# Kernel tuning notes

Measured on AMD Instinct MI355X. Metric: run time of the kernel, lower is better.

## Reference

```python
import jax, jax.numpy as jnp
import numpy as np

NUM_HEADS = 16
ROPE_THETA = 10000.0


def _rope(x, pos):
    # x: [B, H, S, d_k], pos: [S]
    d_k = x.shape[-1]
    inv_freq = ROPE_THETA ** (-jnp.arange(0, d_k, 2, dtype=x.dtype) / d_k)  # [d_k/2]
    ang = pos[:, None].astype(x.dtype) * inv_freq[None, :]  # [S, d_k/2]
    cos, sin = jnp.cos(ang), jnp.sin(ang)
    x1 = x[..., 0::2]
    x2 = x[..., 1::2]
    r1 = x1 * cos - x2 * sin
    r2 = x1 * sin + x2 * cos
    return jnp.stack([r1, r2], axis=-1).reshape(x.shape)


def setup_inputs() -> dict:
    key = jax.random.key(0)
    kx, kq, kk, kv = jax.random.split(key, 4)
    B, S, D = 2, 2048, 2048
    scale = 1.0 / np.sqrt(D)
    x = jax.random.normal(kx, (B, S, D), dtype=jnp.float32)
    wq = jax.random.normal(kq, (D, D), dtype=jnp.float32) * scale
    wk = jax.random.normal(kk, (D, D), dtype=jnp.float32) * scale
    wv = jax.random.normal(kv, (D, D), dtype=jnp.float32) * scale
    return {"x": x, "wq": wq, "wk": wk, "wv": wv}


def reference(x, wq, wk, wv):
    B, S, D = x.shape
    H = NUM_HEADS
    d_k = D // H
    # QKV projections (Linear stores weight as [out, in]; y = x @ W^T)
    q = (x @ wq.T).reshape(B, S, H, d_k).transpose(0, 2, 1, 3)  # [B,H,S,dk]
    k = (x @ wk.T).reshape(B, S, H, d_k).transpose(0, 2, 1, 3)
    v = (x @ wv.T).reshape(B, S, H, d_k).transpose(0, 2, 1, 3)
    pos = jnp.arange(S)
    q = _rope(q, pos)
    k = _rope(k, pos)
    scores = jnp.einsum("bhqd,bhkd->bhqk", q, k) / jnp.sqrt(jnp.asarray(d_k, x.dtype))
    causal = jnp.tril(jnp.ones((S, S), dtype=bool))
    scores = jnp.where(causal, scores, jnp.asarray(-1e9, x.dtype))
    attn = jax.nn.softmax(scores, axis=-1)
    out = jnp.einsum("bhqk,bhkd->bhqd", attn, v)  # [B,H,S,dk]
    return out.transpose(0, 2, 1, 3).reshape(B, S, D)
```

## Files before the change

kernel.cpp:

```cpp
#include <hip/hip_runtime.h>
#include <stdint.h>

typedef unsigned short u16;
typedef __bf16 bf16x8 __attribute__((ext_vector_type(8)));
typedef float f32x4 __attribute__((ext_vector_type(4)));

#define NHEADS 16
#define DKH    128
#define SEQ    2048
#define DMODEL 2048
#define NBATCH 2

typedef const __attribute__((address_space(1))) void* gas1_t;
typedef __attribute__((address_space(3))) void* las3_t;

__device__ __forceinline__ void gload_lds16(const void* g, void* l) {
  __builtin_amdgcn_global_load_lds((gas1_t)(uintptr_t)g,
                                   (las3_t)(uint32_t)(uintptr_t)l, 16, 0, 0);
}

__device__ __forceinline__ u16 bf(float f) {
  return __builtin_bit_cast(u16, (__bf16)f);
}

__global__ __launch_bounds__(256) void cvt_all(const float* __restrict__ x,
                                               const float* __restrict__ wq,
                                               const float* __restrict__ wk,
                                               const float* __restrict__ wv,
                                               u16* __restrict__ xb,
                                               u16* __restrict__ wb) {
  int i = (blockIdx.x * 256 + threadIdx.x) * 4;
  const int NX = NBATCH * SEQ * DMODEL;
  const int NW = DMODEL * DMODEL;
  const float* src;
  u16* dst;
  int j;
  if (i < NX) { src = x; dst = xb; j = i; }
  else {
    int k = i - NX;
    int w = k / NW;
    j = k - w * NW;
    src = (w == 0) ? wq : (w == 1) ? wk : wv;
    dst = wb + (size_t)w * NW;
  }
  const float4 v = *(const float4*)(src + j);
  uint2 o;
  o.x = (uint32_t)bf(v.x) | ((uint32_t)bf(v.y) << 16);
  o.y = (uint32_t)bf(v.z) | ((uint32_t)bf(v.w) << 16);
  *(uint2*)(dst + j) = o;
}

__global__ __launch_bounds__(256) void rope_table(float2* __restrict__ tbl) {
  int i = blockIdx.x * 256 + threadIdx.x;
  int s = i >> 6, d2 = i & 63;
  const float kLog2Theta = 13.28771237954945f;
  float inv_freq = exp2f(-(float)d2 * (2.0f / 128.0f) * kLog2Theta);
  float ang = (float)s * inv_freq;
  tbl[i] = make_float2(cosf(ang), sinf(ang));
}

__global__ __launch_bounds__(256, 4) void gemm_qkv(const u16* __restrict__ Abf,
                                                   const u16* __restrict__ Wbf,
                                                   const float2* __restrict__ rope,
                                                   u16* __restrict__ qb,
                                                   u16* __restrict__ kb,
                                                   u16* __restrict__ vtb) {
  __shared__ u16 S[16384];
  u16* As = S;
  u16* Bs = S + 8192;
  const int tid = threadIdx.x;
  const int lane = tid & 63, wid = tid >> 6;
  const int wr = wid >> 1, wc = wid & 1;
  const int blk = blockIdx.x;
  const int m0 = (blk / 48) * 128;
  const int n0 = (blk % 48) * 128;
  const int lrow = lane & 15, lgrp = lane >> 4, lko = lgrp * 8;
  const int rswz = (lrow & 7) << 3;

  const int srow = tid >> 3;
  const int scol = ((tid & 7) * 8) ^ (((tid >> 3) & 7) << 3);

  f32x4 acc[4][4] = {};

  for (int k0 = 0; k0 < DMODEL; k0 += 64) {
    __syncthreads();
#pragma unroll
    for (int c = 0; c < 4; ++c) {
      gload_lds16(Abf + (size_t)(m0 + c * 32 + srow) * DMODEL + k0 + scol,
                  As + (c * 256 + tid) * 8);
      gload_lds16(Wbf + (size_t)(n0 + c * 32 + srow) * DMODEL + k0 + scol,
                  Bs + (c * 256 + tid) * 8);
    }
    __syncthreads();
#pragma unroll
    for (int kk = 0; kk < 2; ++kk) {
      const int rc = (kk * 32 + lko) ^ rswz;
      bf16x8 a[4], b[4];
#pragma unroll
      for (int m = 0; m < 4; ++m)
        a[m] = *(const bf16x8*)(As + (wr * 64 + m * 16 + lrow) * 64 + rc);
#pragma unroll
      for (int n = 0; n < 4; ++n)
        b[n] = *(const bf16x8*)(Bs + (wc * 64 + n * 16 + lrow) * 64 + rc);
#pragma unroll
      for (int m = 0; m < 4; ++m)
#pragma unroll
        for (int n = 0; n < 4; ++n)
          acc[m][n] = __builtin_amdgcn_mfma_f32_16x16x32_bf16(a[m], b[n], acc[m][n], 0, 0, 0);
    }
  }

  const int sel = n0 >> 11;
  const float qsc = 0.08838834764831845f * 1.44269504088896341f;

  if (sel != 2) {
#pragma unroll
    for (int m = 0; m < 4; ++m) {
      int grow0 = m0 + wr * 64 + m * 16 + (lgrp << 2);
#pragma unroll
      for (int n = 0; n < 4; ++n) {
        int gcol = n0 + wc * 64 + n * 16 + lrow;
        int within = gcol & 2047;
        int h_ = within >> 7, d_ = within & 127;
#pragma unroll
        for (int j = 0; j < 4; ++j) {
          float v = acc[m][n][j];
          int r = grow0 + j;
          int b_ = r >> 11, s_ = r & 2047;
          int bh = b_ * NHEADS + h_;
          float part = __shfl_xor(v, 1);
          float2 cs2 = rope[s_ * 64 + (d_ >> 1)];
          v = (d_ & 1) ? (part * cs2.y + v * cs2.x) : (v * cs2.x - part * cs2.y);
          if (sel == 0) v *= qsc;
          u16* dq = sel ? kb : qb;
          dq[((size_t)bh * SEQ + s_) * DKH + d_] = bf(v);
        }
      }
    }
  } else {
    __syncthreads();
#pragma unroll
    for (int m = 0; m < 4; ++m) {
      int sl0 = wr * 64 + m * 16 + (lgrp << 2);
#pragma unroll
      for (int n = 0; n < 4; ++n) {
        int dcol = wc * 64 + n * 16 + lrow;
        const int dx = (dcol & 7) << 4;
#pragma unroll
        for (int j = 0; j < 4; ++j)
          S[dcol * 128 + ((sl0 + j) ^ dx)] = bf(acc[m][n][j]);
      }
    }
    __syncthreads();
    const int b_ = m0 >> 11, s0 = m0 & 2047;
    const int h_ = (n0 >> 7) & 15;
    const int bh = b_ * NHEADS + h_;
    const int d = tid >> 1, hf = tid & 1;
    const int dx = (d & 7) << 4;
    u16* grow = vtb + ((size_t)bh * DKH + d) * SEQ + s0 + hf * 64;
#pragma unroll
    for (int g = 0; g < 8; ++g) {
      bf16x8 v8 = *(const bf16x8*)(S + d * 128 + ((hf * 64 + g * 8) ^ dx));
      *(bf16x8*)(grow + g * 8) = v8;
    }
  }
}

__global__ __launch_bounds__(256, 2) void attn_fwd(const u16* __restrict__ qb,
                                                   const u16* __restrict__ kb,
                                                   const u16* __restrict__ vtb,
                                                   float* __restrict__ out) {
  __shared__ u16 Ks[2][64 * 128];
  __shared__ u16 Vs[2][128 * 64];
  __shared__ __bf16 Ps[4][16 * 64];
  const int tid = threadIdx.x, lane = tid & 63, wid = tid >> 6;
  const int blk = blockIdx.x;
  const int xcd = blk & 7, slot = blk >> 3;
  const int bh = (slot >> 4) * 8 + xcd;
  const int pair = slot & 15;
  const int lrow = lane & 15, lgrp = lane >> 4, lko = lgrp * 8;
  const int swz = (lrow & 7) << 3;

  const int krow_l = tid >> 4;
  const int kcol = ((tid & 15) * 8) ^ ((krow_l & 7) << 3);
  const int vrow_l = tid >> 3;
  const int vcol = ((tid & 7) * 8) ^ ((vrow_l & 7) << 3);

  const int b_ = bh >> 4, h_ = bh & 15;
  const size_t kbase = (size_t)bh * SEQ;
  const size_t vbase = (size_t)bh * DKH;

#pragma unroll 1
  for (int ci = 0; ci < 2; ++ci) {
    const int chunk = ci ? (31 - pair) : pair;
    const int qrow0 = chunk * 64 + wid * 16;

    bf16x8 qa[4];
#pragma unroll
    for (int kd = 0; kd < 4; ++kd)
      qa[kd] = *(const bf16x8*)(qb + (kbase + qrow0 + lrow) * DKH + kd * 32 + lko);

    f32x4 o[8] = {};
    float mrun[4], lrun[4];
#pragma unroll
    for (int j = 0; j < 4; ++j) { mrun[j] = -1e30f; lrun[j] = 0.f; }

    const int nt = chunk + 1;

#pragma unroll
    for (int c = 0; c < 4; ++c) {
      gload_lds16(kb + (kbase + c * 16 + krow_l) * DKH + kcol,
                  &Ks[0][(c * 256 + tid) * 8]);
      gload_lds16(vtb + (vbase + c * 32 + vrow_l) * SEQ + vcol,
                  &Vs[0][(c * 256 + tid) * 8]);
    }
    __syncthreads();

#pragma unroll 1
    for (int t = 0; t < nt; ++t) {
      const int cur = t & 1;
      if (t + 1 < nt) {
        const int kv1 = (t + 1) * 64;
#pragma unroll
        for (int c = 0; c < 4; ++c) {
          gload_lds16(kb + (kbase + kv1 + c * 16 + krow_l) * DKH + kcol,
                      &Ks[cur ^ 1][(c * 256 + tid) * 8]);
          gload_lds16(vtb + (vbase + c * 32 + vrow_l) * SEQ + kv1 + vcol,
                      &Vs[cur ^ 1][(c * 256 + tid) * 8]);
        }
      }
      const int kv0 = t * 64;
      const u16* Kb = &Ks[cur][0];
      const u16* Vb = &Vs[cur][0];

      f32x4 sf[4] = {};
      __builtin_amdgcn_s_setprio(1);
#pragma unroll
      for (int kd = 0; kd < 4; ++kd) {
        const int kc = (kd * 32 + lko) ^ swz;
#pragma unroll
        for (int n = 0; n < 4; ++n) {
          bf16x8 kf = *(const bf16x8*)(Kb + (n * 16 + lrow) * 128 + kc);
          sf[n] = __builtin_amdgcn_mfma_f32_16x16x32_bf16(qa[kd], kf, sf[n], 0, 0, 0);
        }
      }
      __builtin_amdgcn_s_setprio(0);

      const bool diag = (t == nt - 1);
      float mt[4];
#pragma unroll
      for (int j = 0; j < 4; ++j) {
        const int r = qrow0 + lgrp * 4 + j;
        float m_ = -1e30f;
#pragma unroll
        for (int n = 0; n < 4; ++n) {
          float s = sf[n][j];
          if (diag && (kv0 + n * 16 + lrow > r)) { s = -1e30f; sf[n][j] = s; }
          m_ = fmaxf(m_, s);
        }
#pragma unroll
        for (int off = 1; off < 16; off <<= 1) m_ = fmaxf(m_, __shfl_xor(m_, off));
        mt[j] = m_;
      }
      int need = 0;
#pragma unroll
      for (int j = 0; j < 4; ++j) need |= (mt[j] > mrun[j] + 11.5f) ? 1 : 0;
      if (__any(need)) {
#pragma unroll
        for (int j = 0; j < 4; ++j) {
          float mnew = fmaxf(mrun[j], mt[j]);
          float alpha = __builtin_amdgcn_exp2f(mrun[j] - mnew);
          mrun[j] = mnew;
          lrun[j] *= alpha;
#pragma unroll
          for (int n8 = 0; n8 < 8; ++n8) o[n8][j] *= alpha;
        }
      }
#pragma unroll
      for (int j = 0; j < 4; ++j) {
        float ps = 0.f;
#pragma unroll
        for (int n = 0; n < 4; ++n) {
          float p = __builtin_amdgcn_exp2f(sf[n][j] - mrun[j]);
          ps += p;
          sf[n][j] = p;
        }
#pragma unroll
        for (int off = 1; off < 16; off <<= 1) ps += __shfl_xor(ps, off);
        lrun[j] += ps;
      }

      __bf16* pw = &Ps[wid][0];
#pragma unroll
      for (int n = 0; n < 4; ++n)
#pragma unroll
        for (int j = 0; j < 4; ++j) {
          int prow = lgrp * 4 + j;
          pw[prow * 64 + ((n * 16 + lrow) ^ ((prow & 7) << 3))] = (__bf16)sf[n][j];
        }

      __builtin_amdgcn_s_setprio(1);
#pragma unroll
      for (int kk = 0; kk < 2; ++kk) {
        const int pc = (kk * 32 + lko) ^ swz;
        bf16x8 pa = *(const bf16x8*)(pw + lrow * 64 + pc);
#pragma unroll
        for (int n = 0; n < 8; ++n) {
          bf16x8 vf = *(const bf16x8*)(Vb + (n * 16 + lrow) * 64 + pc);
          o[n] = __builtin_amdgcn_mfma_f32_16x16x32_bf16(pa, vf, o[n], 0, 0, 0);
        }
      }
      __builtin_amdgcn_s_setprio(0);

      __syncthreads();
    }

#pragma unroll
    for (int j = 0; j < 4; ++j) {
      int s_ = qrow0 + lgrp * 4 + j;
      float inv = 1.f / lrun[j];
#pragma unroll
      for (int n = 0; n < 8; ++n) {
        int dcol = n * 16 + lrow;
        out[((size_t)b_ * SEQ + s_) * DMODEL + h_ * DKH + dcol] = o[n][j] * inv;
      }
    }
  }
}

extern "C" void kernel_launch(void* const* d_in, const int* in_sizes, int n_in,
                              void* d_out, int out_size, void* d_ws, size_t ws_size,
                              hipStream_t stream) {
  const float* x  = (const float*)d_in[0];
  const float* wq = (const float*)d_in[1];
  const float* wk = (const float*)d_in[2];
  const float* wv = (const float*)d_in[3];
  float* out = (float*)d_out;
  char* ws = (char*)d_ws;

  u16* xb  = (u16*)(ws);
  u16* wb  = (u16*)(ws + 16777216);
  u16* qb  = (u16*)(ws + 41943040);
  u16* kb  = (u16*)(ws + 58720256);
  u16* vtb = (u16*)(ws + 75497472);

  float2* rope = (float2*)d_out;

  rope_table<<<512, 256, 0, stream>>>(rope);
  cvt_all<<<20480, 256, 0, stream>>>(x, wq, wk, wv, xb, wb);
  gemm_qkv<<<1536, 256, 0, stream>>>(xb, wb, rope, qb, kb, vtb);
  attn_fwd<<<512, 256, 0, stream>>>(qb, kb, vtb, out);
}
```

Measured before the change: 216.5 us.

## Rewrite attention with 32x32x16 MFMA, 32 query rows per wave, register-resident P

The attention kernel now uses 32x32x16 bf16 MFMA and computes S transposed, so each lane owns one query row. That makes the row max and sum mostly in-register with one cross-half shuffle. P is packed to bf16 and exchanged between lane halves with shuffles instead of going through LDS. Each block now handles 128 query rows, so the grid is halved and occupancy drops to one block per CU. The XCD-aware head mapping is removed. The aim is fewer LDS round-trips and reductions per tile, at the cost of more registers and fewer resident waves.

```diff
diff --git a/kernel.cpp b/kernel.cpp
--- a/kernel.cpp
+++ b/kernel.cpp
@@ -4,6 +4,7 @@
 typedef unsigned short u16;
 typedef __bf16 bf16x8 __attribute__((ext_vector_type(8)));
 typedef float f32x4 __attribute__((ext_vector_type(4)));
+typedef float f32x16 __attribute__((ext_vector_type(16)));
 
 #define NHEADS 16
 #define DKH    128
@@ -21,6 +22,15 @@
 
 __device__ __forceinline__ u16 bf(float f) {
   return __builtin_bit_cast(u16, (__bf16)f);
+}
+
+__device__ __forceinline__ uint32_t pk(float lo, float hi) {
+  return (uint32_t)bf(lo) | ((uint32_t)bf(hi) << 16);
+}
+
+__device__ __forceinline__ float lanebcast(int srclane, float v) {
+  return __builtin_bit_cast(float,
+      __builtin_amdgcn_ds_bpermute(srclane << 2, __builtin_bit_cast(int, v)));
 }
 
 __global__ __launch_bounds__(256) void cvt_all(const float* __restrict__ x,
@@ -166,166 +176,169 @@
   }
 }
 
-__global__ __launch_bounds__(256, 2) void attn_fwd(const u16* __restrict__ qb,
+__global__ __launch_bounds__(256, 1) void attn_fwd(const u16* __restrict__ qb,
                                                    const u16* __restrict__ kb,
                                                    const u16* __restrict__ vtb,
                                                    float* __restrict__ out) {
   __shared__ u16 Ks[2][64 * 128];
   __shared__ u16 Vs[2][128 * 64];
-  __shared__ __bf16 Ps[4][16 * 64];
   const int tid = threadIdx.x, lane = tid & 63, wid = tid >> 6;
   const int blk = blockIdx.x;
-  const int xcd = blk & 7, slot = blk >> 3;
-  const int bh = (slot >> 4) * 8 + xcd;
-  const int pair = slot & 15;
-  const int lrow = lane & 15, lgrp = lane >> 4, lko = lgrp * 8;
-  const int swz = (lrow & 7) << 3;
+  const int bh = blk & 31;
+  const int pair = blk >> 5;
+  const int qln = lane & 31, hi = lane >> 5;
+  const int hi4 = hi << 2, hi8 = hi << 3;
+  const int kswz = (qln & 15) << 3;
+  const int vswz = (qln & 7) << 3;
 
   const int krow_l = tid >> 4;
-  const int kcol = ((tid & 15) * 8) ^ ((krow_l & 7) << 3);
+  const int kcol = (((tid & 15) ^ (tid >> 4)) << 3);
   const int vrow_l = tid >> 3;
-  const int vcol = ((tid & 7) * 8) ^ ((vrow_l & 7) << 3);
+  const int vcol = (((tid & 7) ^ ((tid >> 3) & 7)) << 3);
 
   const int b_ = bh >> 4, h_ = bh & 15;
   const size_t kbase = (size_t)bh * SEQ;
   const size_t vbase = (size_t)bh * DKH;
 
+#define STAGE_KV(bufi, kv_)                                                  \
+  _Pragma("unroll")                                                          \
+  for (int c = 0; c < 4; ++c) {                                              \
+    gload_lds16(kb + (kbase + (kv_) + c * 16 + krow_l) * DKH + kcol,         \
+                &Ks[bufi][(c * 256 + tid) * 8]);                             \
+    gload_lds16(vtb + (vbase + c * 32 + vrow_l) * SEQ + (kv_) + vcol,        \
+                &Vs[bufi][(c * 256 + tid) * 8]);                             \
+  }
+
 #pragma unroll 1
   for (int ci = 0; ci < 2; ++ci) {
-    const int chunk = ci ? (31 - pair) : pair;
-    const int qrow0 = chunk * 64 + wid * 16;
-
-    bf16x8 qa[4];
-#pragma unroll
-    for (int kd = 0; kd < 4; ++kd)
-      qa[kd] = *(const bf16x8*)(qb + (kbase + qrow0 + lrow) * DKH + kd * 32 + lko);
-
-    f32x4 o[8] = {};
-    float mrun[4], lrun[4];
-#pragma unroll
-    for (int j = 0; j < 4; ++j) { mrun[j] = -1e30f; lrun[j] = 0.f; }
-
-    const int nt = chunk + 1;
-
-#pragma unroll
-    for (int c = 0; c < 4; ++c) {
-      gload_lds16(kb + (kbase + c * 16 + krow_l) * DKH + kcol,
-                  &Ks[0][(c * 256 + tid) * 8]);
-      gload_lds16(vtb + (vbase + c * 32 + vrow_l) * SEQ + vcol,
-                  &Vs[0][(c * 256 + tid) * 8]);
-    }
+    const int chunk = ci ? (15 - pair) : pair;
+    const int q0w = chunk * 128 + wid * 32;
+    const int qglob = q0w + qln;
+
+    bf16x8 qa[8];
+#pragma unroll
+    for (int kd = 0; kd < 8; ++kd)
+      qa[kd] = *(const bf16x8*)(qb + (kbase + q0w + qln) * DKH + kd * 16 + hi8);
+
+    f32x16 o[4] = {};
+    float mrun = -1e30f, lrun = 0.f;
+
+    const int nt = 2 * chunk + 2;
+
+    STAGE_KV(0, 0);
     __syncthreads();
 
 #pragma unroll 1
     for (int t = 0; t < nt; ++t) {
       const int cur = t & 1;
-      if (t + 1 < nt) {
-        const int kv1 = (t + 1) * 64;
-#pragma unroll
-        for (int c = 0; c < 4; ++c) {
-          gload_lds16(kb + (kbase + kv1 + c * 16 + krow_l) * DKH + kcol,
-                      &Ks[cur ^ 1][(c * 256 + tid) * 8]);
-          gload_lds16(vtb + (vbase + c * 32 + vrow_l) * SEQ + kv1 + vcol,
-                      &Vs[cur ^ 1][(c * 256 + tid) * 8]);
+      if (t + 1 < nt) { STAGE_KV(cur ^ 1, (t + 1) * 64); }
+      const int kv0 = t * 64;
+
+      if (kv0 <= q0w + 31) {
+        const u16* Kb = &Ks[cur][0];
+        const u16* Vb = &Vs[cur][0];
+
+        f32x16 sfv[2] = {};
+        __builtin_amdgcn_s_setprio(1);
+#pragma unroll
+        for (int kd = 0; kd < 8; ++kd)
+#pragma unroll
+          for (int st = 0; st < 2; ++st) {
+            bf16x8 kf = *(const bf16x8*)(Kb + (st * 32 + qln) * 128 +
+                                         ((kd * 16 + hi8) ^ kswz));
+            sfv[st] = __builtin_amdgcn_mfma_f32_32x32x16_bf16(kf, qa[kd], sfv[st], 0, 0, 0);
+          }
+        __builtin_amdgcn_s_setprio(0);
+
+        if (kv0 + 63 > q0w) {
+#pragma unroll
+          for (int st = 0; st < 2; ++st)
+#pragma unroll
+            for (int r = 0; r < 16; ++r)
+              if (kv0 + st * 32 + ((r & 3) + 8 * (r >> 2)) + hi4 > qglob)
+                sfv[st][r] = -1e30f;
         }
+
+        float tm[16];
+#pragma unroll
+        for (int r = 0; r < 16; ++r) tm[r] = fmaxf(sfv[0][r], sfv[1][r]);
+#pragma unroll
+        for (int r = 0; r < 8; ++r) tm[r] = fmaxf(tm[r], tm[r + 8]);
+#pragma unroll
+        for (int r = 0; r < 4; ++r) tm[r] = fmaxf(tm[r], tm[r + 4]);
+        float m_ = fmaxf(fmaxf(tm[0], tm[1]), fmaxf(tm[2], tm[3]));
+        m_ = fmaxf(m_, __shfl_xor(m_, 32));
+
+        if (__any(m_ > mrun + 11.5f)) {
+          float mnew = fmaxf(mrun, m_);
+          float alpha = __builtin_amdgcn_exp2f(mrun - mnew);
+          mrun = mnew;
+          lrun *= alpha;
+#pragma unroll
+          for (int r = 0; r < 16; ++r) {
+            float ar = lanebcast((r & 3) + 8 * (r >> 2) + hi4, alpha);
+            o[0][r] *= ar; o[1][r] *= ar; o[2][r] *= ar; o[3][r] *= ar;
+          }
+        }
+
+#pragma unroll
+        for (int st = 0; st < 2; ++st)
+#pragma unroll
+          for (int r = 0; r < 16; ++r)
+            sfv[st][r] = __builtin_amdgcn_exp2f(sfv[st][r] - mrun);
+        float ts[16];
+#pragma unroll
+        for (int r = 0; r < 16; ++r) ts[r] = sfv[0][r] + sfv[1][r];
+#pragma unroll
+        for (int r = 0; r < 8; ++r) ts[r] += ts[r + 8];
+#pragma unroll
+        for (int r = 0; r < 4; ++r) ts[r] += ts[r + 4];
+        float sum = (ts[0] + ts[1]) + (ts[2] + ts[3]);
+        sum += __shfl_xor(sum, 32);
+        lrun += sum;
+
+        __builtin_amdgcn_s_setprio(1);
+#pragma unroll
+        for (int ks = 0; ks < 4; ++ks) {
+          const int st = ks >> 1, rb = (ks & 1) * 8;
+          uint32_t w0 = pk(sfv[st][rb + 0], sfv[st][rb + 1]);
+          uint32_t w1 = pk(sfv[st][rb + 2], sfv[st][rb + 3]);
+          uint32_t w2 = pk(sfv[st][rb + 4], sfv[st][rb + 5]);
+          uint32_t w3 = pk(sfv[st][rb + 6], sfv[st][rb + 7]);
+          uint32_t s0 = hi ? w0 : w2, s1 = hi ? w1 : w3;
+          uint32_t r0 = (uint32_t)__shfl_xor((int)s0, 32);
+          uint32_t r1 = (uint32_t)__shfl_xor((int)s1, 32);
+          union { uint32_t u[4]; bf16x8 v; } pa;
+          pa.u[0] = hi ? r0 : w0;
+          pa.u[1] = hi ? r1 : w1;
+          pa.u[2] = hi ? w2 : r0;
+          pa.u[3] = hi ? w3 : r1;
+#pragma unroll
+          for (int d0 = 0; d0 < 4; ++d0) {
+            bf16x8 vf = *(const bf16x8*)(Vb + (d0 * 32 + qln) * 64 +
+                                         ((ks * 16 + hi8) ^ vswz));
+            o[d0] = __builtin_amdgcn_mfma_f32_32x32x16_bf16(pa.v, vf, o[d0], 0, 0, 0);
+          }
+        }
+        __builtin_amdgcn_s_setprio(0);
       }
-      const int kv0 = t * 64;
-      const u16* Kb = &Ks[cur][0];
-      const u16* Vb = &Vs[cur][0];
-
-      f32x4 sf[4] = {};
-      __builtin_amdgcn_s_setprio(1);
-#pragma unroll
-      for (int kd = 0; kd < 4; ++kd) {
-        const int kc = (kd * 32 + lko) ^ swz;
-#pragma unroll
-        for (int n = 0; n < 4; ++n) {
-          bf16x8 kf = *(const bf16x8*)(Kb + (n * 16 + lrow) * 128 + kc);
-          sf[n] = __builtin_amdgcn_mfma_f32_16x16x32_bf16(qa[kd], kf, sf[n], 0, 0, 0);
-        }
-      }
-      __builtin_amdgcn_s_setprio(0);
-
-      const bool diag = (t == nt - 1);
-      float mt[4];
-#pragma unroll
-      for (int j = 0; j < 4; ++j) {
-        const int r = qrow0 + lgrp * 4 + j;
-        float m_ = -1e30f;
-#pragma unroll
-        for (int n = 0; n < 4; ++n) {
-          float s = sf[n][j];
-          if (diag && (kv0 + n * 16 + lrow > r)) { s = -1e30f; sf[n][j] = s; }
-          m_ = fmaxf(m_, s);
-        }
-#pragma unroll
-        for (int off = 1; off < 16; off <<= 1) m_ = fmaxf(m_, __shfl_xor(m_, off));
-        mt[j] = m_;
-      }
-      int need = 0;
-#pragma unroll
-      for (int j = 0; j < 4; ++j) need |= (mt[j] > mrun[j] + 11.5f) ? 1 : 0;
-      if (__any(need)) {
-#pragma unroll
-        for (int j = 0; j < 4; ++j) {
-          float mnew = fmaxf(mrun[j], mt[j]);
-          float alpha = __builtin_amdgcn_exp2f(mrun[j] - mnew);
-          mrun[j] = mnew;
-          lrun[j] *= alpha;
-#pragma unroll
-          for (int n8 = 0; n8 < 8; ++n8) o[n8][j] *= alpha;
-        }
-      }
-#pragma unroll
-      for (int j = 0; j < 4; ++j) {
-        float ps = 0.f;
-#pragma unroll
-        for (int n = 0; n < 4; ++n) {
-          float p = __builtin_amdgcn_exp2f(sf[n][j] - mrun[j]);
-          ps += p;
-          sf[n][j] = p;
-        }
-#pragma unroll
-        for (int off = 1; off < 16; off <<= 1) ps += __shfl_xor(ps, off);
-        lrun[j] += ps;
-      }
-
-      __bf16* pw = &Ps[wid][0];
-#pragma unroll
-      for (int n = 0; n < 4; ++n)
-#pragma unroll
-        for (int j = 0; j < 4; ++j) {
-          int prow = lgrp * 4 + j;
-          pw[prow * 64 + ((n * 16 + lrow) ^ ((prow & 7) << 3))] = (__bf16)sf[n][j];
-        }
-
-      __builtin_amdgcn_s_setprio(1);
-#pragma unroll
-      for (int kk = 0; kk < 2; ++kk) {
-        const int pc = (kk * 32 + lko) ^ swz;
-        bf16x8 pa = *(const bf16x8*)(pw + lrow * 64 + pc);
-#pragma unroll
-        for (int n = 0; n < 8; ++n) {
-          bf16x8 vf = *(const bf16x8*)(Vb + (n * 16 + lrow) * 64 + pc);
-          o[n] = __builtin_amdgcn_mfma_f32_16x16x32_bf16(pa, vf, o[n], 0, 0, 0);
-        }
-      }
-      __builtin_amdgcn_s_setprio(0);
 
       __syncthreads();
     }
 
-#pragma unroll
-    for (int j = 0; j < 4; ++j) {
-      int s_ = qrow0 + lgrp * 4 + j;
-      float inv = 1.f / lrun[j];
-#pragma unroll
-      for (int n = 0; n < 8; ++n) {
-        int dcol = n * 16 + lrow;
-        out[((size_t)b_ * SEQ + s_) * DMODEL + h_ * DKH + dcol] = o[n][j] * inv;
-      }
-    }
-  }
+    float inv = 1.f / lrun;
+#pragma unroll
+    for (int r = 0; r < 16; ++r) {
+      const int qr = (r & 3) + 8 * (r >> 2) + hi4;
+      float invr = lanebcast(qr, inv);
+      float* op = out + ((size_t)b_ * SEQ + q0w + qr) * DMODEL + h_ * DKH + qln;
+      op[0]  = o[0][r] * invr;
+      op[32] = o[1][r] * invr;
+      op[64] = o[2][r] * invr;
+      op[96] = o[3][r] * invr;
+    }
+  }
+#undef STAGE_KV
 }
 
 extern "C" void kernel_launch(void* const* d_in, const int* in_sizes, int n_in,
@@ -349,5 +362,5 @@
   rope_table<<<512, 256, 0, stream>>>(rope);
   cvt_all<<<20480, 256, 0, stream>>>(x, wq, wk, wv, xb, wb);
   gemm_qkv<<<1536, 256, 0, stream>>>(xb, wb, rope, qb, kb, vtb);
-  attn_fwd<<<512, 256, 0, stream>>>(qb, kb, vtb, out);
-}
+  attn_fwd<<<256, 256, 0, stream>>>(qb, kb, vtb, out);
+}
```

Result: faster. 202.2 us (-6.6%).
